# Kernel tuning notes

Hardware: AMD Instinct MI355X
Metric: run time of the kernel (lower is better)

The kernel has to match this reference:

```python
import jax, jax.numpy as jnp
import numpy as np

NEG = -1e10


def setup_inputs() -> dict:
    key = jax.random.key(0)
    ks = jax.random.split(key, 16)
    B, ql, TN, al = 16, 32, 10, 10
    V, E, H = 50000, 300, 256
    inp = {
        'q': jax.random.randint(ks[0], (B, ql), 0, V),
        'alia': jax.random.randint(ks[1], (B, TN, al), 0, V),
        'els': jax.random.uniform(ks[2], (B, TN), jnp.float32),
        'elo': jax.random.uniform(ks[3], (B, TN), jnp.float32),
        'cate': jax.random.uniform(ks[4], (B, TN, 2), jnp.float32),
        # learned params
        'emb': jax.random.normal(ks[5], (V, E), jnp.float32),
        'sim_w': jax.random.normal(ks[6], (3 * E, 1), jnp.float32) * 0.02,
        'sim_b': jnp.zeros((1,), jnp.float32),
        'enc_w': jax.random.normal(ks[7], (2 * E, H), jnp.float32) * 0.02,
        'enc_b': jnp.zeros((H,), jnp.float32),
        'qlin_w': jax.random.normal(ks[8], (H, 1), jnp.float32) * 0.02,
        'qlin_b': jnp.zeros((1,), jnp.float32),
        'cls_w': jax.random.normal(ks[9], (5, 1), jnp.float32) * 0.1,
        'cls_b': jnp.zeros((1,), jnp.float32),
    }
    return inp


def reference(q, alia, els, elo, cate, emb, sim_w, sim_b, enc_w, enc_b,
              qlin_w, qlin_b, cls_w, cls_b):
    B, ql = q.shape
    _, TN, al = alia.shape
    E = emb.shape[1]

    # per-forward L2 renormalization of the embedding table, padding row zeroed
    emb_n = emb / jnp.maximum(jnp.linalg.norm(emb, axis=1, keepdims=True), 1e-12)
    emb_n = emb_n.at[0].set(0.0)

    q_emb = emb_n[q]                       # [B, ql, E]
    a_emb = emb_n[alia].reshape(B, TN * al, E)  # [B, TN*al, E]

    q_mask = (q != 0).astype(jnp.float32)                    # [B, ql]
    a_mask = (alia != 0).reshape(B, TN * al).astype(jnp.float32)
    mask = a_mask[:, :, None] * q_mask[:, None, :]           # [B, TN*al, ql]

    # similar([w, v, w*v]) decomposed: w@W1 + v@W2 + (w*v)@W3 + b (same math,
    # avoids materializing the [B,TN*al,ql,3E] concat)
    W1, W2, W3 = sim_w[:E, 0], sim_w[E:2 * E, 0], sim_w[2 * E:, 0]
    atten = (a_emb @ W1)[:, :, None] + (q_emb @ W2)[:, None, :] \
        + jnp.einsum('bme,bqe->bmq', a_emb * W3, q_emb) + sim_b[0]
    atten = mask * atten + (1.0 - mask) * NEG                # [B, TN*al, ql]
    atten4 = atten.reshape(B, TN, al, ql)

    atten1 = jax.nn.softmax(atten4, axis=3).reshape(B, TN * al, ql)
    alig = jnp.einsum('bmq,bqe->bme', atten1, q_emb)          # [B, TN*al, E]

    enc_in = jnp.concatenate([alig, a_emb], axis=-1)          # [B, TN*al, 2E]
    enc = jax.nn.relu(enc_in @ enc_w + enc_b).reshape(B, TN, al, -1)
    compare = enc.sum(axis=2)                                 # [B, TN, H]
    alia_score = compare @ qlin_w + qlin_b                    # [B, TN, 1]

    feats = jnp.concatenate(
        [elo[:, :, None], els[:, :, None], cate, alia_score], axis=2)  # [B,TN,5]
    logits = (feats @ cls_w + cls_b)[:, :, 0]                 # [B, TN]

    tmask = ((els + elo) != 0).astype(jnp.float32)            # [B, TN]
    mask_logits = tmask * logits + (1.0 - tmask) * NEG

    max_atten = jax.lax.stop_gradient(atten4.max(axis=2))     # [B, TN, ql]
    p = jax.nn.softmax(mask_logits, axis=1)[:, :, None]
    atten_out = jax.nn.softmax((p * max_atten).sum(axis=1), axis=1)  # [B, ql]
    return mask_logits, atten_out
```

## Files before the change

### kernel.cpp

```cpp
#include <hip/hip_runtime.h>
#include <math.h>

#define NEGV (-10000000000.0f)

constexpr int B  = 16;
constexpr int QL = 32;
constexpr int TN = 10;
constexpr int AL = 10;
constexpr int E  = 300;
constexpr int H  = 256;
constexpr int M  = TN * AL;
constexpr int NQ = B * QL;
constexpr int NA = B * M;
constexpr int SQS = 304;

constexpr size_t OFF_AEMB = 0;
constexpr size_t OFF_ATT  = OFF_AEMB + (size_t)NA * SQS;
constexpr size_t OFF_P    = OFF_ATT + (size_t)NA * QL;
constexpr size_t OFF_QW   = OFF_P + (size_t)NA * QL;
constexpr size_t OFF_PS   = OFF_QW + (size_t)NQ * H;

__global__ __launch_bounds__(256) void k2_fused(
    const int* __restrict__ q, const int* __restrict__ alia,
    const float* __restrict__ emb,
    const float* __restrict__ sim_w, const float* __restrict__ sim_b,
    const float* __restrict__ enc_w, float* __restrict__ ws) {
  __shared__ float smem[13248];
  int tid = threadIdx.x;
  int wid = tid >> 6, lane = tid & 63;

  if (blockIdx.x < 320) {
    int mh = blockIdx.x & 1, btn = blockIdx.x >> 1;
    int b = btn / TN;
    int bm0 = btn * AL + mh * 5;
    float* sq    = smem;
    float* sa    = smem + 32 * 308;
    float* a3    = smem + 32 * 308 + 5 * 304;
    float* s_qw2 = a3 + 6 * 304;
    float* s_aw1 = s_qw2 + 32;
    float* s_scA = s_aw1 + 8;

    for (int i = tid; i < 32 * 75; i += 256) {
      int r = i / 75, e4 = i % 75;
      int idx = q[b * QL + r];
      *(float4*)&sq[r * 308 + e4 * 4] =
          *(const float4*)&emb[(size_t)idx * E + e4 * 4];
    }
    for (int i = tid; i < 5 * 75; i += 256) {
      int j = i / 75, e4 = i % 75;
      int idx = alia[bm0 + j];
      *(float4*)&sa[j * 304 + e4 * 4] =
          *(const float4*)&emb[(size_t)idx * E + e4 * 4];
    }
    for (int i = tid; i < 304; i += 256) a3[5 * 304 + i] = 0.f;
    __syncthreads();

    for (int r = wid; r < 37; r += 4) {
      bool isa = r >= 32;
      const float* row = isa ? &sa[(r - 32) * 304] : &sq[r * 308];
      const float* W = isa ? sim_w : (sim_w + E);
      float ss = 0.f, dw = 0.f;
      for (int e = lane; e < E; e += 64) {
        float v = row[e];
        ss += v * v;
        dw += v * W[e];
      }
      #pragma unroll
      for (int off = 32; off > 0; off >>= 1) {
        ss += __shfl_xor(ss, off);
        dw += __shfl_xor(dw, off);
      }
      if (lane == 0) {
        int idx = isa ? alia[bm0 + (r - 32)] : q[b * QL + r];
        float scale = (idx == 0) ? 0.f : (1.f / fmaxf(sqrtf(ss), 1e-12f));
        if (isa) { s_scA[r - 32] = scale; s_aw1[r - 32] = dw * scale; }
        else s_qw2[r] = dw * scale;
      }
    }
    __syncthreads();

    const float* w3 = sim_w + 2 * E;
    for (int i = tid; i < 5 * 75; i += 256) {
      int j = i / 75, e4 = i % 75;
      float sc = s_scA[j];
      float4 v = *(const float4*)&sa[j * 304 + e4 * 4];
      float4 wv = *(const float4*)&w3[e4 * 4];
      float4 vn; vn.x = v.x*sc; vn.y = v.y*sc; vn.z = v.z*sc; vn.w = v.w*sc;
      *(float4*)&ws[OFF_AEMB + (size_t)(bm0 + j) * SQS + e4 * 4] = vn;
      float4 a3v; a3v.x = vn.x*wv.x; a3v.y = vn.y*wv.y;
      a3v.z = vn.z*wv.z; a3v.w = vn.w*wv.w;
      *(float4*)&a3[j * 304 + e4 * 4] = a3v;
    }
    __syncthreads();

    if (wid < 3) {
      int g = lane & 31, l = lane >> 5;
      int m = wid * 2 + l;
      float simb = sim_b[0];
      const float* qr = &sq[g * 308];
      const float* ar = &a3[m * 304];
      float acc = 0.f;
      for (int e4 = 0; e4 < 75; ++e4) {
        float4 qv = *(const float4*)&qr[e4 * 4];
        float4 av = *(const float4*)&ar[e4 * 4];
        acc += av.x*qv.x + av.y*qv.y + av.z*qv.z + av.w*qv.w;
      }
      if (m < 5) {
        int bm = bm0 + m;
        float att = s_aw1[m] + s_qw2[g] + acc + simb;
        if (!(alia[bm] != 0 && q[b * QL + g] != 0)) att = NEGV;
        ws[OFF_ATT + (size_t)bm * QL + g] = att;
        float mx = att;
        #pragma unroll
        for (int off = 1; off < 32; off <<= 1) mx = fmaxf(mx, __shfl_xor(mx, off));
        float ex = expf(att - mx);
        float sm = ex;
        #pragma unroll
        for (int off = 1; off < 32; off <<= 1) sm += __shfl_xor(sm, off);
        ws[OFF_P + (size_t)bm * QL + g] = ex / sm;
      }
    }
  } else {
    int rg = blockIdx.x - 320;
    int nh = rg & 1, rgi = rg >> 1;
    int slot0 = rgi * 8;
    float* sQ = smem;
    float* spart = smem + 8 * 304;
    float* s_scB = spart + 8192;

    for (int i = tid; i < 8 * 75; i += 256) {
      int r = i / 75, e4 = i % 75;
      int idx = q[slot0 + r];
      *(float4*)&sQ[r * 304 + e4 * 4] =
          *(const float4*)&emb[(size_t)idx * E + e4 * 4];
    }
    __syncthreads();
    for (int r = wid; r < 8; r += 4) {
      const float* row = &sQ[r * 304];
      float ss = 0.f;
      for (int e = lane; e < E; e += 64) { float v = row[e]; ss += v * v; }
      #pragma unroll
      for (int off = 32; off > 0; off >>= 1) ss += __shfl_xor(ss, off);
      if (lane == 0) {
        int idx = q[slot0 + r];
        s_scB[r] = (idx == 0) ? 0.f : (1.f / fmaxf(sqrtf(ss), 1e-12f));
      }
    }
    __syncthreads();

    int c = tid & 31, kq = tid >> 5;
    int ks = kq * 40;
    int nch = (kq == 7) ? 5 : 10;
    float acc[8][4] = {};
    for (int ch = 0; ch < nch; ++ch) {
      int k = ks + ch * 4;
      float4 a[8];
      #pragma unroll
      for (int j = 0; j < 8; j++) a[j] = *(const float4*)&sQ[j * 304 + k];
      const float* wp = enc_w + (size_t)k * H + nh * 128 + c;
      #pragma unroll
      for (int e = 0; e < 4; e++) {
        float w0 = wp[e * H + 0];
        float w1 = wp[e * H + 32];
        float w2 = wp[e * H + 64];
        float w3v = wp[e * H + 96];
        #pragma unroll
        for (int j = 0; j < 8; j++) {
          float av = (e == 0) ? a[j].x : (e == 1) ? a[j].y
                   : (e == 2) ? a[j].z : a[j].w;
          acc[j][0] += av * w0; acc[j][1] += av * w1;
          acc[j][2] += av * w2; acc[j][3] += av * w3v;
        }
      }
    }
    #pragma unroll
    for (int j = 0; j < 8; j++)
      #pragma unroll
      for (int nc = 0; nc < 4; nc++)
        spart[((kq * 8 + j) * 4 + nc) * 32 + c] = acc[j][nc];
    __syncthreads();
    #pragma unroll
    for (int t = 0; t < 4; t++) {
      int o = tid + t * 256;
      int j = o >> 7, colh = o & 127;
      float s = 0.f;
      #pragma unroll
      for (int kk = 0; kk < 8; kk++)
        s += spart[((kk * 8 + j) * 4 + (colh >> 5)) * 32 + (colh & 31)];
      ws[OFF_QW + (size_t)(slot0 + j) * H + nh * 128 + colh] = s * s_scB[j];
    }
  }
}

__global__ __launch_bounds__(256) void k2b_enc(
    const float* __restrict__ enc_w, const float* __restrict__ enc_b,
    const float* __restrict__ qlin_w, float* __restrict__ ws) {
  int blk = blockIdx.x;
  int nh = blk & 1, jh = (blk >> 1) & 1, btn = blk >> 2;
  int b = btn / TN;
  int tid = threadIdx.x;
  int c = tid & 31, kq = tid >> 5;
  int bm0 = btn * AL + jh * 5;

  __shared__ float sA[5 * 304];
  __shared__ float sP[5 * 32];
  __shared__ float spart[8 * 5 * 4 * 32];
  __shared__ float s_red[2];

  const float* ga = ws + OFF_AEMB + (size_t)bm0 * SQS;
  for (int i = tid; i < 5 * 75; i += 256) {
    int j = i / 75, e4 = i % 75;
    *(float4*)&sA[j * 304 + e4 * 4] = *(const float4*)&ga[j * SQS + e4 * 4];
  }
  if (tid < 160) sP[tid] = ws[OFF_P + (size_t)bm0 * QL + tid];
  __syncthreads();

  float acc[5][4] = {};

  {
    float4 pv[5];
    #pragma unroll
    for (int j = 0; j < 5; j++) pv[j] = *(const float4*)&sP[j * 32 + kq * 4];
    const float* qwb = ws + OFF_QW + (size_t)(b * QL + kq * 4) * H + nh * 128 + c;
    #pragma unroll
    for (int pp = 0; pp < 4; pp++) {
      float w0 = qwb[pp * H + 0];
      float w1 = qwb[pp * H + 32];
      float w2 = qwb[pp * H + 64];
      float w3v = qwb[pp * H + 96];
      #pragma unroll
      for (int j = 0; j < 5; j++) {
        float p = (pp == 0) ? pv[j].x : (pp == 1) ? pv[j].y
                : (pp == 2) ? pv[j].z : pv[j].w;
        acc[j][0] += p * w0; acc[j][1] += p * w1;
        acc[j][2] += p * w2; acc[j][3] += p * w3v;
      }
    }
  }

  int ks = kq * 40;
  int nch = (kq == 7) ? 5 : 10;
  for (int ch = 0; ch < nch; ++ch) {
    int k = ks + ch * 4;
    float4 a[5];
    #pragma unroll
    for (int j = 0; j < 5; j++) a[j] = *(const float4*)&sA[j * 304 + k];
    const float* wp = enc_w + (size_t)(E + k) * H + nh * 128 + c;
    #pragma unroll
    for (int e = 0; e < 4; e++) {
      float w0 = wp[e * H + 0];
      float w1 = wp[e * H + 32];
      float w2 = wp[e * H + 64];
      float w3v = wp[e * H + 96];
      #pragma unroll
      for (int j = 0; j < 5; j++) {
        float av = (e == 0) ? a[j].x : (e == 1) ? a[j].y
                 : (e == 2) ? a[j].z : a[j].w;
        acc[j][0] += av * w0; acc[j][1] += av * w1;
        acc[j][2] += av * w2; acc[j][3] += av * w3v;
      }
    }
  }

  #pragma unroll
  for (int j = 0; j < 5; j++)
    #pragma unroll
    for (int nc = 0; nc < 4; nc++)
      spart[((kq * 5 + j) * 4 + nc) * 32 + c] = acc[j][nc];
  __syncthreads();

  float v = 0.f;
  if (tid < 128) {
    int colh = tid, col = nh * 128 + colh;
    float bias = enc_b[col];
    float s = 0.f;
    #pragma unroll
    for (int j = 0; j < 5; j++) {
      float t = bias;
      #pragma unroll
      for (int kk = 0; kk < 8; kk++)
        t += spart[((kk * 5 + j) * 4 + (colh >> 5)) * 32 + (colh & 31)];
      s += fmaxf(t, 0.f);
    }
    v = s * qlin_w[col];
  }
  #pragma unroll
  for (int off = 32; off > 0; off >>= 1) v += __shfl_down(v, off);
  if (tid < 128 && (tid & 63) == 0) s_red[tid >> 6] = v;
  __syncthreads();
  if (tid == 0) ws[OFF_PS + blk] = s_red[0] + s_red[1];
}

__global__ __launch_bounds__(256) void k3_final(
    const float* __restrict__ els, const float* __restrict__ elo,
    const float* __restrict__ cate, const float* __restrict__ qlin_b,
    const float* __restrict__ cls_w, const float* __restrict__ cls_b,
    const float* __restrict__ ws, float* __restrict__ out) {
  int b = blockIdx.x;
  int tid = threadIdx.x;
  __shared__ float s_logit[TN], s_p[TN];
  __shared__ float s_at[M * QL];

  const float* attb = ws + OFF_ATT + (size_t)b * M * QL;
  for (int i = tid; i < 800; i += 256)
    *(float4*)&s_at[i * 4] = *(const float4*)&attb[i * 4];

  if (tid < TN) {
    const float* ps = ws + OFF_PS + (size_t)(b * TN + tid) * 4;
    float score = ps[0] + ps[1] + ps[2] + ps[3] + qlin_b[0];
    float lo = elo[b * TN + tid], ls = els[b * TN + tid];
    float c0 = cate[(b * TN + tid) * 2 + 0];
    float c1 = cate[(b * TN + tid) * 2 + 1];
    float logit = lo * cls_w[0] + ls * cls_w[1] + c0 * cls_w[2] +
                  c1 * cls_w[3] + score * cls_w[4] + cls_b[0];
    s_logit[tid] = ((ls + lo) != 0.0f) ? logit : NEGV;
  }
  __syncthreads();

  if (tid == 0) {
    float mx = -INFINITY;
    for (int t = 0; t < TN; t++) mx = fmaxf(mx, s_logit[t]);
    float sm = 0.f;
    for (int t = 0; t < TN; t++) sm += expf(s_logit[t] - mx);
    for (int t = 0; t < TN; t++) s_p[t] = expf(s_logit[t] - mx) / sm;
  }
  if (tid < TN) out[b * TN + tid] = s_logit[tid];
  __syncthreads();

  if (tid < QL) {
    float sacc = 0.f;
    for (int tn2 = 0; tn2 < TN; tn2++) {
      float mxa = -INFINITY;
      #pragma unroll
      for (int al = 0; al < AL; al++) {
        mxa = fmaxf(mxa, s_at[(tn2 * AL + al) * QL + tid]);
      }
      sacc += s_p[tn2] * mxa;
    }
    float mx = sacc;
    #pragma unroll
    for (int off = 16; off > 0; off >>= 1) mx = fmaxf(mx, __shfl_xor(mx, off, 32));
    float ex = expf(sacc - mx);
    float sm = ex;
    #pragma unroll
    for (int off = 16; off > 0; off >>= 1) sm += __shfl_xor(sm, off, 32);
    out[B * TN + b * QL + tid] = ex / sm;
  }
}

extern "C" void kernel_launch(void* const* d_in, const int* in_sizes, int n_in,
                              void* d_out, int out_size, void* d_ws, size_t ws_size,
                              hipStream_t stream) {
  const int*   q      = (const int*)  d_in[0];
  const int*   alia   = (const int*)  d_in[1];
  const float* els    = (const float*)d_in[2];
  const float* elo    = (const float*)d_in[3];
  const float* cate   = (const float*)d_in[4];
  const float* emb    = (const float*)d_in[5];
  const float* sim_w  = (const float*)d_in[6];
  const float* sim_b  = (const float*)d_in[7];
  const float* enc_w  = (const float*)d_in[8];
  const float* enc_b  = (const float*)d_in[9];
  const float* qlin_w = (const float*)d_in[10];
  const float* qlin_b = (const float*)d_in[11];
  const float* cls_w  = (const float*)d_in[12];
  const float* cls_b  = (const float*)d_in[13];
  float* out = (float*)d_out;
  float* ws  = (float*)d_ws;

  k2_fused<<<320 + 128, 256, 0, stream>>>(q, alia, emb, sim_w, sim_b, enc_w, ws);
  k2b_enc<<<B * TN * 4, 256, 0, stream>>>(enc_w, enc_b, qlin_w, ws);
  k3_final<<<B, 256, 0, stream>>>(els, elo, cate, qlin_b, cls_w, cls_b, ws, out);
}
```

Measured before the change: 34.93 us.

## Fuse final softmax kernel into encoder via last-block atomic counter; vectorize weight loads

Removes the separate k3_final launch: each k2b_enc block increments a per-batch atomic counter, and the last block for a batch computes logits and the attention-output softmax, reusing spart as shared scratch. A memset of the counters is added before the kernels. The enc_w and qw loads are also changed to float4 per thread, with each thread owning 4 contiguous columns, and the spart layout is adjusted to match. This trades one kernel launch for an extra memset call plus threadfence and atomic overhead, and the float4 column layout may change LDS bank conflict behavior.

```diff
diff --git a/kernel.cpp b/kernel.cpp
--- a/kernel.cpp
+++ b/kernel.cpp
@@ -19,6 +19,7 @@
 constexpr size_t OFF_P    = OFF_ATT + (size_t)NA * QL;
 constexpr size_t OFF_QW   = OFF_P + (size_t)NA * QL;
 constexpr size_t OFF_PS   = OFF_QW + (size_t)NQ * H;
+constexpr size_t OFF_CNT  = OFF_PS + 640;
 
 __global__ __launch_bounds__(256) void k2_fused(
     const int* __restrict__ q, const int* __restrict__ alia,
@@ -157,27 +158,24 @@
       float4 a[8];
       #pragma unroll
       for (int j = 0; j < 8; j++) a[j] = *(const float4*)&sQ[j * 304 + k];
-      const float* wp = enc_w + (size_t)k * H + nh * 128 + c;
+      const float* wp = enc_w + (size_t)k * H + nh * 128 + c * 4;
       #pragma unroll
       for (int e = 0; e < 4; e++) {
-        float w0 = wp[e * H + 0];
-        float w1 = wp[e * H + 32];
-        float w2 = wp[e * H + 64];
-        float w3v = wp[e * H + 96];
+        float4 wv = *(const float4*)&wp[e * H];
         #pragma unroll
         for (int j = 0; j < 8; j++) {
           float av = (e == 0) ? a[j].x : (e == 1) ? a[j].y
                    : (e == 2) ? a[j].z : a[j].w;
-          acc[j][0] += av * w0; acc[j][1] += av * w1;
-          acc[j][2] += av * w2; acc[j][3] += av * w3v;
+          acc[j][0] += av * wv.x; acc[j][1] += av * wv.y;
+          acc[j][2] += av * wv.z; acc[j][3] += av * wv.w;
         }
       }
     }
     #pragma unroll
-    for (int j = 0; j < 8; j++)
-      #pragma unroll
-      for (int nc = 0; nc < 4; nc++)
-        spart[((kq * 8 + j) * 4 + nc) * 32 + c] = acc[j][nc];
+    for (int j = 0; j < 8; j++) {
+      float4 t; t.x = acc[j][0]; t.y = acc[j][1]; t.z = acc[j][2]; t.w = acc[j][3];
+      *(float4*)&spart[((kq * 8 + j) * 32 + c) * 4] = t;
+    }
     __syncthreads();
     #pragma unroll
     for (int t = 0; t < 4; t++) {
@@ -186,7 +184,7 @@
       float s = 0.f;
       #pragma unroll
       for (int kk = 0; kk < 8; kk++)
-        s += spart[((kk * 8 + j) * 4 + (colh >> 5)) * 32 + (colh & 31)];
+        s += spart[((kk * 8 + j) * 32 + (colh >> 2)) * 4 + (colh & 3)];
       ws[OFF_QW + (size_t)(slot0 + j) * H + nh * 128 + colh] = s * s_scB[j];
     }
   }
@@ -194,7 +192,11 @@
 
 __global__ __launch_bounds__(256) void k2b_enc(
     const float* __restrict__ enc_w, const float* __restrict__ enc_b,
-    const float* __restrict__ qlin_w, float* __restrict__ ws) {
+    const float* __restrict__ qlin_w, const float* __restrict__ qlin_b,
+    const float* __restrict__ els, const float* __restrict__ elo,
+    const float* __restrict__ cate,
+    const float* __restrict__ cls_w, const float* __restrict__ cls_b,
+    float* __restrict__ ws, float* __restrict__ out) {
   int blk = blockIdx.x;
   int nh = blk & 1, jh = (blk >> 1) & 1, btn = blk >> 2;
   int b = btn / TN;
@@ -204,8 +206,10 @@
 
   __shared__ float sA[5 * 304];
   __shared__ float sP[5 * 32];
-  __shared__ float spart[8 * 5 * 4 * 32];
+  __shared__ float spart[8 * 5 * 32 * 4];
   __shared__ float s_red[2];
+  __shared__ float s_logit[TN], s_pb[TN];
+  __shared__ unsigned s_old;
 
   const float* ga = ws + OFF_AEMB + (size_t)bm0 * SQS;
   for (int i = tid; i < 5 * 75; i += 256) {
@@ -221,19 +225,16 @@
     float4 pv[5];
     #pragma unroll
     for (int j = 0; j < 5; j++) pv[j] = *(const float4*)&sP[j * 32 + kq * 4];
-    const float* qwb = ws + OFF_QW + (size_t)(b * QL + kq * 4) * H + nh * 128 + c;
+    const float* qwb = ws + OFF_QW + (size_t)(b * QL + kq * 4) * H + nh * 128 + c * 4;
     #pragma unroll
     for (int pp = 0; pp < 4; pp++) {
-      float w0 = qwb[pp * H + 0];
-      float w1 = qwb[pp * H + 32];
-      float w2 = qwb[pp * H + 64];
-      float w3v = qwb[pp * H + 96];
+      float4 wv = *(const float4*)&qwb[pp * H];
       #pragma unroll
       for (int j = 0; j < 5; j++) {
         float p = (pp == 0) ? pv[j].x : (pp == 1) ? pv[j].y
                 : (pp == 2) ? pv[j].z : pv[j].w;
-        acc[j][0] += p * w0; acc[j][1] += p * w1;
-        acc[j][2] += p * w2; acc[j][3] += p * w3v;
+        acc[j][0] += p * wv.x; acc[j][1] += p * wv.y;
+        acc[j][2] += p * wv.z; acc[j][3] += p * wv.w;
       }
     }
   }
@@ -245,28 +246,25 @@
     float4 a[5];
     #pragma unroll
     for (int j = 0; j < 5; j++) a[j] = *(const float4*)&sA[j * 304 + k];
-    const float* wp = enc_w + (size_t)(E + k) * H + nh * 128 + c;
+    const float* wp = enc_w + (size_t)(E + k) * H + nh * 128 + c * 4;
     #pragma unroll
     for (int e = 0; e < 4; e++) {
-      float w0 = wp[e * H + 0];
-      float w1 = wp[e * H + 32];
-      float w2 = wp[e * H + 64];
-      float w3v = wp[e * H + 96];
+      float4 wv = *(const float4*)&wp[e * H];
       #pragma unroll
       for (int j = 0; j < 5; j++) {
         float av = (e == 0) ? a[j].x : (e == 1) ? a[j].y
                  : (e == 2) ? a[j].z : a[j].w;
-        acc[j][0] += av * w0; acc[j][1] += av * w1;
-        acc[j][2] += av * w2; acc[j][3] += av * w3v;
+        acc[j][0] += av * wv.x; acc[j][1] += av * wv.y;
+        acc[j][2] += av * wv.z; acc[j][3] += av * wv.w;
       }
     }
   }
 
   #pragma unroll
-  for (int j = 0; j < 5; j++)
-    #pragma unroll
-    for (int nc = 0; nc < 4; nc++)
-      spart[((kq * 5 + j) * 4 + nc) * 32 + c] = acc[j][nc];
+  for (int j = 0; j < 5; j++) {
+    float4 t; t.x = acc[j][0]; t.y = acc[j][1]; t.z = acc[j][2]; t.w = acc[j][3];
+    *(float4*)&spart[((kq * 5 + j) * 32 + c) * 4] = t;
+  }
   __syncthreads();
 
   float v = 0.f;
@@ -279,7 +277,7 @@
       float t = bias;
       #pragma unroll
       for (int kk = 0; kk < 8; kk++)
-        t += spart[((kk * 5 + j) * 4 + (colh >> 5)) * 32 + (colh & 31)];
+        t += spart[((kk * 5 + j) * 32 + (colh >> 2)) * 4 + (colh & 3)];
       s += fmaxf(t, 0.f);
     }
     v = s * qlin_w[col];
@@ -288,19 +286,16 @@
   for (int off = 32; off > 0; off >>= 1) v += __shfl_down(v, off);
   if (tid < 128 && (tid & 63) == 0) s_red[tid >> 6] = v;
   __syncthreads();
-  if (tid == 0) ws[OFF_PS + blk] = s_red[0] + s_red[1];
-}
-
-__global__ __launch_bounds__(256) void k3_final(
-    const float* __restrict__ els, const float* __restrict__ elo,
-    const float* __restrict__ cate, const float* __restrict__ qlin_b,
-    const float* __restrict__ cls_w, const float* __restrict__ cls_b,
-    const float* __restrict__ ws, float* __restrict__ out) {
-  int b = blockIdx.x;
-  int tid = threadIdx.x;
-  __shared__ float s_logit[TN], s_p[TN];
-  __shared__ float s_at[M * QL];
-
+  if (tid == 0) {
+    ws[OFF_PS + blk] = s_red[0] + s_red[1];
+    __threadfence();
+    s_old = atomicAdd((unsigned*)(ws + OFF_CNT) + b, 1u);
+  }
+  __syncthreads();
+  if (s_old != 4 * TN - 1) return;
+
+  __threadfence();
+  float* s_at = spart;
   const float* attb = ws + OFF_ATT + (size_t)b * M * QL;
   for (int i = tid; i < 800; i += 256)
     *(float4*)&s_at[i * 4] = *(const float4*)&attb[i * 4];
@@ -322,7 +317,7 @@
     for (int t = 0; t < TN; t++) mx = fmaxf(mx, s_logit[t]);
     float sm = 0.f;
     for (int t = 0; t < TN; t++) sm += expf(s_logit[t] - mx);
-    for (int t = 0; t < TN; t++) s_p[t] = expf(s_logit[t] - mx) / sm;
+    for (int t = 0; t < TN; t++) s_pb[t] = expf(s_logit[t] - mx) / sm;
   }
   if (tid < TN) out[b * TN + tid] = s_logit[tid];
   __syncthreads();
@@ -335,7 +330,7 @@
       for (int al = 0; al < AL; al++) {
         mxa = fmaxf(mxa, s_at[(tn2 * AL + al) * QL + tid]);
       }
-      sacc += s_p[tn2] * mxa;
+      sacc += s_pb[tn2] * mxa;
     }
     float mx = sacc;
     #pragma unroll
@@ -368,7 +363,9 @@
   float* out = (float*)d_out;
   float* ws  = (float*)d_ws;
 
+  hipMemsetAsync((char*)d_ws + OFF_CNT * sizeof(float), 0, B * sizeof(unsigned),
+                 stream);
   k2_fused<<<320 + 128, 256, 0, stream>>>(q, alia, emb, sim_w, sim_b, enc_w, ws);
-  k2b_enc<<<B * TN * 4, 256, 0, stream>>>(enc_w, enc_b, qlin_w, ws);
-  k3_final<<<B, 256, 0, stream>>>(els, elo, cate, qlin_b, cls_w, cls_b, ws, out);
+  k2b_enc<<<B * TN * 4, 256, 0, stream>>>(enc_w, enc_b, qlin_w, qlin_b,
+                                          els, elo, cate, cls_w, cls_b, ws, out);
 }
```

New measurement: 53.71 us. 53.8% more time.
